# Performance work log

Hardware: AMD Instinct MI355X
Metric: run time of the kernel (lower is better)

## Reference

```python
import jax, jax.numpy as jnp
import numpy as np

B, N, OBS = 512, 64, 256
H1, H2 = 4, 4
D = 128            # embed/key dim (d_k_1 = d_k_2 = 128)
O1 = D // H1       # 32, per-head value dim stage 1
O2 = D // H2       # 32, per-head value dim stage 2
IN2 = O1 * H1      # 128, input dim to stage 2
FOUT = 16          # final_output_dim


def setup_inputs() -> dict:
    key = jax.random.key(0)
    ks = jax.random.split(key, 22)
    g = lambda k, shp: (jax.random.normal(k, shp, dtype=jnp.float32) * 0.05)
    inp = {
        "states": jax.random.normal(ks[0], (B, N, OBS), dtype=jnp.float32),
        # stage 1 per-head params, stacked over heads
        "E1_w": g(ks[1], (H1, D, OBS)), "E1_b": g(ks[2], (H1, D)),
        "K1_w": g(ks[3], (H1, D, D)),   "K1_b": g(ks[4], (H1, D)),
        "Q1_w": g(ks[5], (H1, D, D)),   "Q1_b": g(ks[6], (H1, D)),
        "V1_w": g(ks[7], (H1, O1, D)),  "V1_b": g(ks[8], (H1, O1)),
        # stage 2 per-head params
        "E2_w": g(ks[9], (H2, D, IN2)), "E2_b": g(ks[10], (H2, D)),
        "K2_w": g(ks[11], (H2, D, D)),  "K2_b": g(ks[12], (H2, D)),
        "Q2_w": g(ks[13], (H2, D, D)),  "Q2_b": g(ks[14], (H2, D)),
        "V2_w": g(ks[15], (H2, O2, D)), "V2_b": g(ks[16], (H2, O2)),
        # final MLP policy head
        "F1_w": g(ks[17], (64, O2 * H2)), "F1_b": g(ks[18], (64,)),
        "F2_w": g(ks[19], (FOUT, 64)),    "F2_b": g(ks[20], (FOUT,)),
    }
    return inp


def _attn_block(x, Ew, Eb, Kw, Kb, Qw, Qb, Vw, Vb, d_k):
    # x: [B,N,I]; all head loops batched via leading head axis h
    se = jax.nn.leaky_relu(jnp.einsum('bni,hdi->hbnd', x, Ew) + Eb[:, None, None, :])  # [h,B,N,D]
    k = jnp.einsum('hbnd,hed->hbne', se, Kw) + Kb[:, None, None, :]
    q = jnp.einsum('hbnd,hed->hbne', se, Qw) + Qb[:, None, None, :]
    w = jax.nn.softmax(jnp.einsum('hbne,hbme->hbnm', q, k) / jnp.sqrt(jnp.float32(d_k)), axis=-1)  # [h,B,N,N]
    v = jax.nn.leaky_relu(jnp.einsum('hbnd,hod->hbno', se, Vw) + Vb[:, None, None, :])  # [h,B,N,O]
    att = jnp.einsum('hbnm,hbmo->hbno', w, v)
    h, b, n, o = att.shape
    return jnp.transpose(att, (1, 2, 0, 3)).reshape(b, n, h * o), w


def reference(states, E1_w, E1_b, K1_w, K1_b, Q1_w, Q1_b, V1_w, V1_b,
              E2_w, E2_b, K2_w, K2_b, Q2_w, Q2_b, V2_w, V2_b,
              F1_w, F1_b, F2_w, F2_b):
    x1, w1 = _attn_block(states, E1_w, E1_b, K1_w, K1_b, Q1_w, Q1_b, V1_w, V1_b, D)
    x2, w2 = _attn_block(x1, E2_w, E2_b, K2_w, K2_b, Q2_w, Q2_b, V2_w, V2_b, D)
    h = jax.nn.leaky_relu(jnp.einsum('bnf,of->bno', x2, F1_w) + F1_b)
    policy = jax.nn.softmax(jnp.einsum('bno,po->bnp', h, F2_w) + F2_b, axis=-1)
    return policy, w1, w2
```

## Files before the change

kernel.cpp:

```cpp
#include <hip/hip_runtime.h>

typedef __attribute__((ext_vector_type(8))) short short8;
typedef __attribute__((ext_vector_type(4))) short short4v;
typedef __attribute__((ext_vector_type(4))) float f32x4;

#define MFMA(a, b, c) __builtin_amdgcn_mfma_f32_16x16x32_bf16((a), (b), (c), 0, 0, 0)

__device__ __forceinline__ short f2bf(float f) {
    union { float f; unsigned u; } v; v.f = f;
    unsigned r = v.u + 0x7fffu + ((v.u >> 16) & 1u);
    return (short)(r >> 16);
}
__device__ __forceinline__ float bf2f(short s) {
    union { unsigned u; float f; } v; v.u = ((unsigned)(unsigned short)s) << 16; return v.f;
}

struct ConvArgs { const float* src[10]; int end[10]; };

__global__ __launch_bounds__(256) void convert_weights_kernel(ConvArgs a, short* __restrict__ dst) {
    int i4 = blockIdx.x * 256 + threadIdx.x;
    int seg = 0;
#pragma unroll
    for (int s = 0; s < 9; s++) seg += (i4 >= a.end[s]) ? 1 : 0;
    int base = (seg == 0) ? 0 : a.end[seg - 1];
    float4 v = ((const float4*)a.src[seg])[i4 - base];
    short4v o; o.x = f2bf(v.x); o.y = f2bf(v.y); o.z = f2bf(v.z); o.w = f2bf(v.w);
    *(short4v*)(dst + (size_t)i4 * 4) = o;
}

#define KQ_LD  136
#define VT_LD  72
#define W_LD   72
#define OFF_K  0
#define OFF_Q  8704
#define OFF_SE 17408
#define OFF_VT 17408
#define OFF_W  8704
#define W32_LD 68
#define SMEM_SHORTS 26112

template<int IN, bool XF32>
__global__ __launch_bounds__(256, 3) void attn_stage_kernel(
    const void* __restrict__ xin,
    const short* __restrict__ Ew, const float* __restrict__ Eb,
    const short* __restrict__ Kw, const float* __restrict__ Kb,
    const short* __restrict__ Qw, const float* __restrict__ Qb,
    const short* __restrict__ Vw, const float* __restrict__ Vb,
    float* __restrict__ w_out,
    short* __restrict__ x_out)
{
    __shared__ short sm[SMEM_SHORTS];
    const int tid  = threadIdx.x;
    const int b    = blockIdx.x & 511;
    const int h    = blockIdx.x >> 9;
    const int wv   = tid >> 6;
    const int lane = tid & 63;
    const int quad = lane >> 4;
    const int l16  = lane & 15;
    const int XLD  = IN + 8;
    constexpr int NK1 = IN / 32;

    if constexpr (XF32) {
        const float* xb = (const float*)xin + (size_t)b * 64 * IN;
#pragma unroll
        for (int r = 0; r < IN / 16; r++) {
            int f4 = tid + 256 * r;
            int row = f4 / (IN / 4), c4 = f4 % (IN / 4);
            float4 v = ((const float4*)xb)[f4];
            short4v o; o.x = f2bf(v.x); o.y = f2bf(v.y); o.z = f2bf(v.z); o.w = f2bf(v.w);
            *(short4v*)&sm[row * XLD + c4 * 4] = o;
        }
    } else {
        const short* xb = (const short*)xin + (size_t)b * 64 * IN;
#pragma unroll
        for (int r = 0; r < IN / 32; r++) {
            int f8 = tid + 256 * r;
            int row = f8 / (IN / 8), c8 = f8 % (IN / 8);
            short8 v = *(const short8*)(xb + (size_t)f8 * 8);
            *(short8*)&sm[row * XLD + c8 * 8] = v;
        }
    }

    short8 ebf[NK1 * 2];
    {
        const short* ewh = Ew + (size_t)h * 128 * IN;
#pragma unroll
        for (int k0i = 0; k0i < NK1; k0i++)
#pragma unroll
            for (int j = 0; j < 2; j++)
                ebf[k0i * 2 + j] = *(const short8*)(ewh + (size_t)(wv * 32 + j * 16 + l16) * IN + k0i * 32 + quad * 8);
    }
    __syncthreads();

    short8 kbf[8];

    {
        f32x4 acc[4][2];
#pragma unroll
        for (int j = 0; j < 2; j++) {
            float bv = Eb[h * 128 + wv * 32 + j * 16 + l16];
            f32x4 c = {bv, bv, bv, bv};
#pragma unroll
            for (int i = 0; i < 4; i++) acc[i][j] = c;
        }
#pragma unroll
        for (int k0i = 0; k0i < NK1; k0i++) {
            short8 a[4];
#pragma unroll
            for (int i = 0; i < 4; i++)
                a[i] = *(const short8*)&sm[(i * 16 + l16) * XLD + k0i * 32 + quad * 8];
#pragma unroll
            for (int i = 0; i < 4; i++)
#pragma unroll
                for (int j = 0; j < 2; j++)
                    acc[i][j] = MFMA(a[i], ebf[k0i * 2 + j], acc[i][j]);
        }
        {
            const short* kwh = Kw + (size_t)h * 128 * 128;
#pragma unroll
            for (int k0i = 0; k0i < 4; k0i++)
#pragma unroll
                for (int j = 0; j < 2; j++)
                    kbf[k0i * 2 + j] = *(const short8*)(kwh + (size_t)(wv * 32 + j * 16 + l16) * 128 + k0i * 32 + quad * 8);
        }
#pragma unroll
        for (int i = 0; i < 4; i++)
#pragma unroll
            for (int j = 0; j < 2; j++)
#pragma unroll
                for (int r = 0; r < 4; r++) {
                    float v = acc[i][j][r];
                    v = (v >= 0.f) ? v : 0.01f * v;
                    sm[OFF_SE + (i * 16 + quad * 4 + r) * KQ_LD + wv * 32 + j * 16 + l16] = f2bf(v);
                }
    }
    __syncthreads();

    f32x4 vacc[2];
    {
        short8 qbf[8];
        const short* qwh = Qw + (size_t)h * 128 * 128;
#pragma unroll
        for (int k0i = 0; k0i < 4; k0i++)
#pragma unroll
            for (int j = 0; j < 2; j++)
                qbf[k0i * 2 + j] = *(const short8*)(qwh + (size_t)(wv * 32 + j * 16 + l16) * 128 + k0i * 32 + quad * 8);
        f32x4 kacc[4][2], qacc[4][2];
#pragma unroll
        for (int j = 0; j < 2; j++) {
            float kb = Kb[h * 128 + wv * 32 + j * 16 + l16];
            float qb = Qb[h * 128 + wv * 32 + j * 16 + l16];
            f32x4 kc = {kb, kb, kb, kb}, qc = {qb, qb, qb, qb};
#pragma unroll
            for (int i = 0; i < 4; i++) { kacc[i][j] = kc; qacc[i][j] = qc; }
        }
#pragma unroll
        for (int k0i = 0; k0i < 4; k0i++) {
            short8 a[4];
#pragma unroll
            for (int i = 0; i < 4; i++)
                a[i] = *(const short8*)&sm[OFF_SE + (i * 16 + l16) * KQ_LD + k0i * 32 + quad * 8];
#pragma unroll
            for (int i = 0; i < 4; i++)
#pragma unroll
                for (int j = 0; j < 2; j++) {
                    kacc[i][j] = MFMA(a[i], kbf[k0i * 2 + j], kacc[i][j]);
                    qacc[i][j] = MFMA(a[i], qbf[k0i * 2 + j], qacc[i][j]);
                }
        }
#pragma unroll
        for (int i = 0; i < 4; i++)
#pragma unroll
            for (int j = 0; j < 2; j++)
#pragma unroll
                for (int r = 0; r < 4; r++) {
                    int row = i * 16 + quad * 4 + r, col = wv * 32 + j * 16 + l16;
                    sm[OFF_K + row * KQ_LD + col] = f2bf(kacc[i][j][r]);
                    sm[OFF_Q + row * KQ_LD + col] = f2bf(qacc[i][j][r]);
                }
        const short* vwh = Vw + (size_t)h * 32 * 128;
        const int n0v = (wv >> 1) * 16, mrow = (wv & 1) * 32;
        short8 vbf[4];
#pragma unroll
        for (int k0i = 0; k0i < 4; k0i++)
            vbf[k0i] = *(const short8*)(vwh + (size_t)(n0v + l16) * 128 + k0i * 32 + quad * 8);
        float vb = Vb[h * 32 + n0v + l16];
        vacc[0] = (f32x4){vb, vb, vb, vb}; vacc[1] = vacc[0];
#pragma unroll
        for (int k0i = 0; k0i < 4; k0i++) {
            short8 a0 = *(const short8*)&sm[OFF_SE + (mrow + l16) * KQ_LD + k0i * 32 + quad * 8];
            short8 a1 = *(const short8*)&sm[OFF_SE + (mrow + 16 + l16) * KQ_LD + k0i * 32 + quad * 8];
            vacc[0] = MFMA(a0, vbf[k0i], vacc[0]);
            vacc[1] = MFMA(a1, vbf[k0i], vacc[1]);
        }
    }
    __syncthreads();

    {
        const int n0v = (wv >> 1) * 16, mrow = (wv & 1) * 32;
#pragma unroll
        for (int i = 0; i < 2; i++)
#pragma unroll
            for (int r = 0; r < 4; r++) {
                float v = vacc[i][r];
                v = (v >= 0.f) ? v : 0.01f * v;
                sm[OFF_VT + (n0v + l16) * VT_LD + mrow + i * 16 + quad * 4 + r] = f2bf(v);
            }
    }

    f32x4 lacc[4];
#pragma unroll
    for (int jj = 0; jj < 4; jj++) lacc[jj] = (f32x4){0.f, 0.f, 0.f, 0.f};
#pragma unroll
    for (int k0 = 0; k0 < 128; k0 += 32) {
        short8 a = *(const short8*)&sm[OFF_Q + (wv * 16 + l16) * KQ_LD + k0 + quad * 8];
#pragma unroll
        for (int jj = 0; jj < 4; jj++) {
            short8 b8 = *(const short8*)&sm[OFF_K + (jj * 16 + l16) * KQ_LD + k0 + quad * 8];
            lacc[jj] = MFMA(a, b8, lacc[jj]);
        }
    }
    __syncthreads();

    {
        const float scale = 0.08838834764831845f;
        float* w32 = (float*)sm;
        float mx[4], inv[4];
#pragma unroll
        for (int r = 0; r < 4; r++) {
            float m = lacc[0][r];
#pragma unroll
            for (int jj = 1; jj < 4; jj++) m = fmaxf(m, lacc[jj][r]);
#pragma unroll
            for (int s = 1; s < 16; s <<= 1) m = fmaxf(m, __shfl_xor(m, s, 16));
            mx[r] = m;
        }
        float sum[4] = {0.f, 0.f, 0.f, 0.f};
#pragma unroll
        for (int jj = 0; jj < 4; jj++)
#pragma unroll
            for (int r = 0; r < 4; r++) {
                float e = __expf((lacc[jj][r] - mx[r]) * scale);
                lacc[jj][r] = e; sum[r] += e;
            }
#pragma unroll
        for (int r = 0; r < 4; r++) {
#pragma unroll
            for (int s = 1; s < 16; s <<= 1) sum[r] += __shfl_xor(sum[r], s, 16);
            inv[r] = 1.0f / sum[r];
        }
#pragma unroll
        for (int r = 0; r < 4; r++) {
            int row = wv * 16 + quad * 4 + r;
#pragma unroll
            for (int jj = 0; jj < 4; jj++) {
                float wval = lacc[jj][r] * inv[r];
                w32[row * W32_LD + jj * 16 + l16] = wval;
                sm[OFF_W + row * W_LD + jj * 16 + l16] = f2bf(wval);
            }
        }
    }
    __syncthreads();

    {
        const float* w32 = (const float*)sm;
        float* wbase = w_out + ((size_t)(h * 512 + b)) * 64 * 64;
#pragma unroll
        for (int s = 0; s < 4; s++) {
            int idx = tid + 256 * s;
            int row = idx >> 4, c4 = (idx & 15) * 4;
            f32x4 v = *(const f32x4*)&w32[row * W32_LD + c4];
            __builtin_nontemporal_store(v, (f32x4*)(wbase + idx * 4));
        }
    }

    {
        f32x4 aacc[2]; aacc[0] = (f32x4){0.f, 0.f, 0.f, 0.f}; aacc[1] = aacc[0];
#pragma unroll
        for (int k0 = 0; k0 < 64; k0 += 32) {
            short8 a = *(const short8*)&sm[OFF_W + (wv * 16 + l16) * W_LD + k0 + quad * 8];
#pragma unroll
            for (int j = 0; j < 2; j++) {
                short8 b8 = *(const short8*)&sm[OFF_VT + (j * 16 + l16) * VT_LD + k0 + quad * 8];
                aacc[j] = MFMA(a, b8, aacc[j]);
            }
        }
        short* xob = x_out + (size_t)b * 64 * 128;
#pragma unroll
        for (int j = 0; j < 2; j++)
#pragma unroll
            for (int r = 0; r < 4; r++)
                xob[(size_t)(wv * 16 + quad * 4 + r) * 128 + h * 32 + j * 16 + l16] = f2bf(aacc[j][r]);
    }
}

#define H_LD 72
__global__ __launch_bounds__(256)
void final_mlp_mfma_kernel(const short* __restrict__ x2,
                           const short* __restrict__ F1wb,
                           const float* __restrict__ F1b,
                           const short* __restrict__ F2wb,
                           const float* __restrict__ F2b,
                           float* __restrict__ policy)
{
    __shared__ short hsm[4][16 * H_LD];
    const int tid  = threadIdx.x;
    const int wv   = tid >> 6;
    const int lane = tid & 63;
    const int quad = lane >> 4;
    const int l16  = lane & 15;
    const int rowbase = blockIdx.x * 64 + wv * 16;

    short8 a[4];
    const short* xrow = x2 + (size_t)(rowbase + l16) * 128;
#pragma unroll
    for (int k = 0; k < 4; k++) a[k] = *(const short8*)(xrow + k * 32 + quad * 8);
    f32x4 acc[4];
#pragma unroll
    for (int j = 0; j < 4; j++) { float bv = F1b[j * 16 + l16]; acc[j] = (f32x4){bv, bv, bv, bv}; }
#pragma unroll
    for (int k = 0; k < 4; k++)
#pragma unroll
        for (int j = 0; j < 4; j++) {
            short8 b8 = *(const short8*)(F1wb + (size_t)(j * 16 + l16) * 128 + k * 32 + quad * 8);
            acc[j] = MFMA(a[k], b8, acc[j]);
        }
    short* hh = &hsm[wv][0];
#pragma unroll
    for (int j = 0; j < 4; j++)
#pragma unroll
        for (int r = 0; r < 4; r++) {
            float v = acc[j][r];
            v = (v >= 0.f) ? v : 0.01f * v;
            hh[(quad * 4 + r) * H_LD + j * 16 + l16] = f2bf(v);
        }
    __syncthreads();

    f32x4 lg;
    { float bv = F2b[l16]; lg = (f32x4){bv, bv, bv, bv}; }
#pragma unroll
    for (int k = 0; k < 2; k++) {
        short8 a2 = *(const short8*)(hh + l16 * H_LD + k * 32 + quad * 8);
        short8 b8 = *(const short8*)(F2wb + (size_t)l16 * 64 + k * 32 + quad * 8);
        lg = MFMA(a2, b8, lg);
    }
#pragma unroll
    for (int r = 0; r < 4; r++) {
        float m = lg[r];
        m = fmaxf(m, __shfl_xor(m, 1, 16));
        m = fmaxf(m, __shfl_xor(m, 2, 16));
        m = fmaxf(m, __shfl_xor(m, 4, 16));
        m = fmaxf(m, __shfl_xor(m, 8, 16));
        float e = __expf(lg[r] - m);
        float s = e;
        s += __shfl_xor(s, 1, 16);
        s += __shfl_xor(s, 2, 16);
        s += __shfl_xor(s, 4, 16);
        s += __shfl_xor(s, 8, 16);
        policy[(size_t)(rowbase + quad * 4 + r) * 16 + l16] = e / s;
    }
}

extern "C" void kernel_launch(void* const* d_in, const int* in_sizes, int n_in,
                              void* d_out, int out_size, void* d_ws, size_t ws_size,
                              hipStream_t stream) {
    const float* states = (const float*)d_in[0];
    const float* E1w = (const float*)d_in[1];  const float* E1b = (const float*)d_in[2];
    const float* K1w = (const float*)d_in[3];  const float* K1b = (const float*)d_in[4];
    const float* Q1w = (const float*)d_in[5];  const float* Q1b = (const float*)d_in[6];
    const float* V1w = (const float*)d_in[7];  const float* V1b = (const float*)d_in[8];
    const float* E2w = (const float*)d_in[9];  const float* E2b = (const float*)d_in[10];
    const float* K2w = (const float*)d_in[11]; const float* K2b = (const float*)d_in[12];
    const float* Q2w = (const float*)d_in[13]; const float* Q2b = (const float*)d_in[14];
    const float* V2w = (const float*)d_in[15]; const float* V2b = (const float*)d_in[16];
    const float* F1w = (const float*)d_in[17]; const float* F1b = (const float*)d_in[18];
    const float* F2w = (const float*)d_in[19]; const float* F2b = (const float*)d_in[20];

    float* out    = (float*)d_out;
    float* policy = out;
    float* w1     = out + 512 * 64 * 16;
    float* w2     = w1 + 4 * 512 * 64 * 64;

    short* wsb = (short*)d_ws;
    short* x1b = wsb;
    short* x2b = wsb + 4194304;
    short* wts = wsb + 8388608;
    short* wE1 = wts;            short* wK1 = wts + 131072;
    short* wQ1 = wts + 196608;   short* wV1 = wts + 262144;
    short* wE2 = wts + 278528;   short* wK2 = wts + 344064;
    short* wQ2 = wts + 409600;   short* wV2 = wts + 475136;
    short* wF1 = wts + 491520;   short* wF2 = wts + 499712;

    ConvArgs ca;
    ca.src[0] = E1w; ca.src[1] = K1w; ca.src[2] = Q1w; ca.src[3] = V1w;
    ca.src[4] = E2w; ca.src[5] = K2w; ca.src[6] = Q2w; ca.src[7] = V2w;
    ca.src[8] = F1w; ca.src[9] = F2w;
    ca.end[0] = 32768;  ca.end[1] = 49152;  ca.end[2] = 65536;  ca.end[3] = 69632;
    ca.end[4] = 86016;  ca.end[5] = 102400; ca.end[6] = 118784; ca.end[7] = 122880;
    ca.end[8] = 124928; ca.end[9] = 125184;
    convert_weights_kernel<<<489, 256, 0, stream>>>(ca, wts);

    attn_stage_kernel<256, true><<<2048, 256, 0, stream>>>(
        (const void*)states, wE1, E1b, wK1, K1b, wQ1, Q1b, wV1, V1b, w1, x1b);
    attn_stage_kernel<128, false><<<2048, 256, 0, stream>>>(
        (const void*)x1b, wE2, E2b, wK2, K2b, wQ2, Q2b, wV2, V2b, w2, x2b);
    final_mlp_mfma_kernel<<<512, 256, 0, stream>>>(x2b, wF1, F1b, wF2, F2b, policy);
}
```

Before: 219.3 us.

## Fold K and Q projections into a single precomputed Kw^T·Qw matrix per head

Precomputes M = Kw^T Qw (plus a Qb·Kw row) per head in a prep kernel, so logits become (se·M^T)·se^T plus a per-key bias term. Terms that are constant per query row (Kb, and Qb·Kb) are dropped because softmax cancels them. This removes one of the two 128x128 projections and the separate K/Q shared-memory buffers. Shared memory drops enough to raise occupancy from 3 to 4 blocks per CU. The cost is a serial fp32 matrix product in the prep kernel and extra bf16 rounding of the fused matrix, which can change numerical accuracy.

```diff
diff --git a/kernel.cpp b/kernel.cpp
--- a/kernel.cpp
+++ b/kernel.cpp
@@ -15,36 +15,75 @@
     union { unsigned u; float f; } v; v.u = ((unsigned)(unsigned short)s) << 16; return v.f;
 }
 
-struct ConvArgs { const float* src[10]; int end[10]; };
-
-__global__ __launch_bounds__(256) void convert_weights_kernel(ConvArgs a, short* __restrict__ dst) {
-    int i4 = blockIdx.x * 256 + threadIdx.x;
-    int seg = 0;
-#pragma unroll
-    for (int s = 0; s < 9; s++) seg += (i4 >= a.end[s]) ? 1 : 0;
-    int base = (seg == 0) ? 0 : a.end[seg - 1];
-    float4 v = ((const float4*)a.src[seg])[i4 - base];
-    short4v o; o.x = f2bf(v.x); o.y = f2bf(v.y); o.z = f2bf(v.z); o.w = f2bf(v.w);
-    *(short4v*)(dst + (size_t)i4 * 4) = o;
-}
-
-#define KQ_LD  136
+struct PrepArgs {
+    const float* csrc[6]; int cend[6];
+    const float* K1w; const float* Q1w; const float* Q1b;
+    const float* K2w; const float* Q2w; const float* Q2b;
+};
+
+__global__ __launch_bounds__(256) void prep_kernel(PrepArgs a, short* __restrict__ dstW,
+                                                   short* __restrict__ M1, short* __restrict__ M2) {
+    const int blk = blockIdx.x, t = threadIdx.x;
+    if (blk < 233) {
+        int i4 = blk * 256 + t;
+        int seg = 0;
+#pragma unroll
+        for (int s = 0; s < 5; s++) seg += (i4 >= a.cend[s]) ? 1 : 0;
+        int base = (seg == 0) ? 0 : a.cend[seg - 1];
+        float4 v = ((const float4*)a.csrc[seg])[i4 - base];
+        short4v o; o.x = f2bf(v.x); o.y = f2bf(v.y); o.z = f2bf(v.z); o.w = f2bf(v.w);
+        *(short4v*)(dstW + (size_t)i4 * 4) = o;
+    } else {
+        int mi = blk - 233;
+        int mat = mi / 9, rg = mi % 9;
+        int s = mat >> 2, h = mat & 3;
+        const float* Kw = s ? a.K2w : a.K1w;
+        const float* Qw = s ? a.Q2w : a.Q1w;
+        const float* Qb = s ? a.Q2b : a.Q1b;
+        short* Mt = (s ? M2 : M1) + h * 144 * 128;
+        int r  = rg * 16 + (t >> 4);
+        int d0 = (t & 15) * 8;
+        float acc[8];
+#pragma unroll
+        for (int j = 0; j < 8; j++) acc[j] = 0.f;
+        const float* kw = Kw + (size_t)h * 16384;
+        if (r < 128) {
+            const float* qw = Qw + (size_t)h * 16384;
+            for (int e = 0; e < 128; e++) {
+                float kv = kw[e * 128 + r];
+                const float* q = qw + e * 128 + d0;
+#pragma unroll
+                for (int j = 0; j < 8; j++) acc[j] = fmaf(kv, q[j], acc[j]);
+            }
+        } else if (r == 128) {
+            const float* qb = Qb + h * 128;
+            for (int e = 0; e < 128; e++) {
+                float qv = qb[e];
+                const float* kk = kw + e * 128 + d0;
+#pragma unroll
+                for (int j = 0; j < 8; j++) acc[j] = fmaf(qv, kk[j], acc[j]);
+            }
+        }
+#pragma unroll
+        for (int j = 0; j < 8; j++) Mt[r * 128 + d0 + j] = f2bf(acc[j]);
+    }
+}
+
+#define SE_LD  136
+#define T_LD   136
 #define VT_LD  72
 #define W_LD   72
-#define OFF_K  0
-#define OFF_Q  8704
-#define OFF_SE 17408
-#define OFF_VT 17408
-#define OFF_W  8704
 #define W32_LD 68
-#define SMEM_SHORTS 26112
+#define R1     8704
+#define R2     17408
+#define D2OFF  19712
+#define SMEM_SHORTS 19840
 
 template<int IN, bool XF32>
-__global__ __launch_bounds__(256, 3) void attn_stage_kernel(
+__global__ __launch_bounds__(256, 4) void attn_stage_kernel(
     const void* __restrict__ xin,
     const short* __restrict__ Ew, const float* __restrict__ Eb,
-    const short* __restrict__ Kw, const float* __restrict__ Kb,
-    const short* __restrict__ Qw, const float* __restrict__ Qb,
+    const short* __restrict__ Mt,
     const short* __restrict__ Vw, const float* __restrict__ Vb,
     float* __restrict__ w_out,
     short* __restrict__ x_out)
@@ -57,27 +96,28 @@
     const int lane = tid & 63;
     const int quad = lane >> 4;
     const int l16  = lane & 15;
-    const int XLD  = IN + 8;
-    constexpr int NK1 = IN / 32;
+    constexpr int NK1   = IN / 32;
+    constexpr int XLD   = IN + 8;
+    constexpr int XBASE = XF32 ? 0 : R1;
 
     if constexpr (XF32) {
         const float* xb = (const float*)xin + (size_t)b * 64 * IN;
 #pragma unroll
-        for (int r = 0; r < IN / 16; r++) {
+        for (int r = 0; r < 16; r++) {
             int f4 = tid + 256 * r;
-            int row = f4 / (IN / 4), c4 = f4 % (IN / 4);
+            int row = f4 >> 6, c4 = (f4 & 63) * 4;
             float4 v = ((const float4*)xb)[f4];
             short4v o; o.x = f2bf(v.x); o.y = f2bf(v.y); o.z = f2bf(v.z); o.w = f2bf(v.w);
-            *(short4v*)&sm[row * XLD + c4 * 4] = o;
+            *(short4v*)&sm[row * XLD + c4] = o;
         }
     } else {
         const short* xb = (const short*)xin + (size_t)b * 64 * IN;
 #pragma unroll
-        for (int r = 0; r < IN / 32; r++) {
+        for (int r = 0; r < 4; r++) {
             int f8 = tid + 256 * r;
-            int row = f8 / (IN / 8), c8 = f8 % (IN / 8);
+            int row = f8 >> 4, c8 = (f8 & 15) * 8;
             short8 v = *(const short8*)(xb + (size_t)f8 * 8);
-            *(short8*)&sm[row * XLD + c8 * 8] = v;
+            *(short8*)&sm[XBASE + row * 136 + c8] = v;
         }
     }
 
@@ -92,7 +132,7 @@
     }
     __syncthreads();
 
-    short8 kbf[8];
+    short8 mbf[8], xbf[4], vbf[4];
 
     {
         f32x4 acc[4][2];
@@ -108,7 +148,7 @@
             short8 a[4];
 #pragma unroll
             for (int i = 0; i < 4; i++)
-                a[i] = *(const short8*)&sm[(i * 16 + l16) * XLD + k0i * 32 + quad * 8];
+                a[i] = *(const short8*)&sm[XBASE + (i * 16 + l16) * XLD + k0i * 32 + quad * 8];
 #pragma unroll
             for (int i = 0; i < 4; i++)
 #pragma unroll
@@ -116,13 +156,17 @@
                     acc[i][j] = MFMA(a[i], ebf[k0i * 2 + j], acc[i][j]);
         }
         {
-            const short* kwh = Kw + (size_t)h * 128 * 128;
-#pragma unroll
-            for (int k0i = 0; k0i < 4; k0i++)
+            const short* mth = Mt + (size_t)h * 144 * 128;
+#pragma unroll
+            for (int k0i = 0; k0i < 4; k0i++) {
 #pragma unroll
                 for (int j = 0; j < 2; j++)
-                    kbf[k0i * 2 + j] = *(const short8*)(kwh + (size_t)(wv * 32 + j * 16 + l16) * 128 + k0i * 32 + quad * 8);
-        }
+                    mbf[k0i * 2 + j] = *(const short8*)(mth + (size_t)(wv * 32 + j * 16 + l16) * 128 + k0i * 32 + quad * 8);
+                xbf[k0i] = *(const short8*)(mth + (size_t)(128 + l16) * 128 + k0i * 32 + quad * 8);
+                vbf[k0i] = *(const short8*)(Vw + (size_t)h * 32 * 128 + (size_t)(((wv >> 1) * 16) + l16) * 128 + k0i * 32 + quad * 8);
+            }
+        }
+        if constexpr (XF32) __syncthreads();
 #pragma unroll
         for (int i = 0; i < 4; i++)
 #pragma unroll
@@ -131,92 +175,86 @@
                 for (int r = 0; r < 4; r++) {
                     float v = acc[i][j][r];
                     v = (v >= 0.f) ? v : 0.01f * v;
-                    sm[OFF_SE + (i * 16 + quad * 4 + r) * KQ_LD + wv * 32 + j * 16 + l16] = f2bf(v);
+                    sm[(i * 16 + quad * 4 + r) * SE_LD + wv * 32 + j * 16 + l16] = f2bf(v);
                 }
     }
     __syncthreads();
 
-    f32x4 vacc[2];
-    {
-        short8 qbf[8];
-        const short* qwh = Qw + (size_t)h * 128 * 128;
-#pragma unroll
-        for (int k0i = 0; k0i < 4; k0i++)
-#pragma unroll
-            for (int j = 0; j < 2; j++)
-                qbf[k0i * 2 + j] = *(const short8*)(qwh + (size_t)(wv * 32 + j * 16 + l16) * 128 + k0i * 32 + quad * 8);
-        f32x4 kacc[4][2], qacc[4][2];
-#pragma unroll
-        for (int j = 0; j < 2; j++) {
-            float kb = Kb[h * 128 + wv * 32 + j * 16 + l16];
-            float qb = Qb[h * 128 + wv * 32 + j * 16 + l16];
-            f32x4 kc = {kb, kb, kb, kb}, qc = {qb, qb, qb, qb};
-#pragma unroll
-            for (int i = 0; i < 4; i++) { kacc[i][j] = kc; qacc[i][j] = qc; }
+    {
+        f32x4 tacc[4][2], dacc[4];
+#pragma unroll
+        for (int i = 0; i < 4; i++) {
+#pragma unroll
+            for (int j = 0; j < 2; j++) tacc[i][j] = (f32x4){0.f, 0.f, 0.f, 0.f};
+            dacc[i] = (f32x4){0.f, 0.f, 0.f, 0.f};
         }
 #pragma unroll
         for (int k0i = 0; k0i < 4; k0i++) {
             short8 a[4];
 #pragma unroll
             for (int i = 0; i < 4; i++)
-                a[i] = *(const short8*)&sm[OFF_SE + (i * 16 + l16) * KQ_LD + k0i * 32 + quad * 8];
+                a[i] = *(const short8*)&sm[(i * 16 + l16) * SE_LD + k0i * 32 + quad * 8];
 #pragma unroll
             for (int i = 0; i < 4; i++)
 #pragma unroll
-                for (int j = 0; j < 2; j++) {
-                    kacc[i][j] = MFMA(a[i], kbf[k0i * 2 + j], kacc[i][j]);
-                    qacc[i][j] = MFMA(a[i], qbf[k0i * 2 + j], qacc[i][j]);
-                }
+                for (int j = 0; j < 2; j++)
+                    tacc[i][j] = MFMA(a[i], mbf[k0i * 2 + j], tacc[i][j]);
+            if (wv == 0) {
+#pragma unroll
+                for (int i = 0; i < 4; i++) dacc[i] = MFMA(a[i], xbf[k0i], dacc[i]);
+            }
         }
 #pragma unroll
         for (int i = 0; i < 4; i++)
 #pragma unroll
             for (int j = 0; j < 2; j++)
 #pragma unroll
-                for (int r = 0; r < 4; r++) {
-                    int row = i * 16 + quad * 4 + r, col = wv * 32 + j * 16 + l16;
-                    sm[OFF_K + row * KQ_LD + col] = f2bf(kacc[i][j][r]);
-                    sm[OFF_Q + row * KQ_LD + col] = f2bf(qacc[i][j][r]);
-                }
-        const short* vwh = Vw + (size_t)h * 32 * 128;
+                for (int r = 0; r < 4; r++)
+                    sm[R1 + (i * 16 + quad * 4 + r) * T_LD + wv * 32 + j * 16 + l16] = f2bf(tacc[i][j][r]);
+        if (wv == 0 && l16 == 0) {
+            float* d2f = (float*)&sm[D2OFF];
+#pragma unroll
+            for (int i = 0; i < 4; i++)
+#pragma unroll
+                for (int r = 0; r < 4; r++)
+                    d2f[i * 16 + quad * 4 + r] = dacc[i][r];
+        }
         const int n0v = (wv >> 1) * 16, mrow = (wv & 1) * 32;
-        short8 vbf[4];
-#pragma unroll
-        for (int k0i = 0; k0i < 4; k0i++)
-            vbf[k0i] = *(const short8*)(vwh + (size_t)(n0v + l16) * 128 + k0i * 32 + quad * 8);
         float vb = Vb[h * 32 + n0v + l16];
-        vacc[0] = (f32x4){vb, vb, vb, vb}; vacc[1] = vacc[0];
+        f32x4 vacc[2]; vacc[0] = (f32x4){vb, vb, vb, vb}; vacc[1] = vacc[0];
 #pragma unroll
         for (int k0i = 0; k0i < 4; k0i++) {
-            short8 a0 = *(const short8*)&sm[OFF_SE + (mrow + l16) * KQ_LD + k0i * 32 + quad * 8];
-            short8 a1 = *(const short8*)&sm[OFF_SE + (mrow + 16 + l16) * KQ_LD + k0i * 32 + quad * 8];
+            short8 a0 = *(const short8*)&sm[(mrow + l16) * SE_LD + k0i * 32 + quad * 8];
+            short8 a1 = *(const short8*)&sm[(mrow + 16 + l16) * SE_LD + k0i * 32 + quad * 8];
             vacc[0] = MFMA(a0, vbf[k0i], vacc[0]);
             vacc[1] = MFMA(a1, vbf[k0i], vacc[1]);
         }
-    }
-    __syncthreads();
-
-    {
-        const int n0v = (wv >> 1) * 16, mrow = (wv & 1) * 32;
 #pragma unroll
         for (int i = 0; i < 2; i++)
 #pragma unroll
             for (int r = 0; r < 4; r++) {
                 float v = vacc[i][r];
                 v = (v >= 0.f) ? v : 0.01f * v;
-                sm[OFF_VT + (n0v + l16) * VT_LD + mrow + i * 16 + quad * 4 + r] = f2bf(v);
-            }
-    }
-
+                sm[R2 + (n0v + l16) * VT_LD + mrow + i * 16 + quad * 4 + r] = f2bf(v);
+            }
+    }
+    __syncthreads();
+
+    float d2v[4];
+    {
+        const float* d2f = (const float*)&sm[D2OFF];
+#pragma unroll
+        for (int jj = 0; jj < 4; jj++) d2v[jj] = d2f[jj * 16 + l16];
+    }
     f32x4 lacc[4];
 #pragma unroll
     for (int jj = 0; jj < 4; jj++) lacc[jj] = (f32x4){0.f, 0.f, 0.f, 0.f};
 #pragma unroll
     for (int k0 = 0; k0 < 128; k0 += 32) {
-        short8 a = *(const short8*)&sm[OFF_Q + (wv * 16 + l16) * KQ_LD + k0 + quad * 8];
+        short8 a = *(const short8*)&sm[R1 + (wv * 16 + l16) * T_LD + k0 + quad * 8];
 #pragma unroll
         for (int jj = 0; jj < 4; jj++) {
-            short8 b8 = *(const short8*)&sm[OFF_K + (jj * 16 + l16) * KQ_LD + k0 + quad * 8];
+            short8 b8 = *(const short8*)&sm[(jj * 16 + l16) * SE_LD + k0 + quad * 8];
             lacc[jj] = MFMA(a, b8, lacc[jj]);
         }
     }
@@ -225,6 +263,10 @@
     {
         const float scale = 0.08838834764831845f;
         float* w32 = (float*)sm;
+#pragma unroll
+        for (int jj = 0; jj < 4; jj++)
+#pragma unroll
+            for (int r = 0; r < 4; r++) lacc[jj][r] += d2v[jj];
         float mx[4], inv[4];
 #pragma unroll
         for (int r = 0; r < 4; r++) {
@@ -256,7 +298,7 @@
             for (int jj = 0; jj < 4; jj++) {
                 float wval = lacc[jj][r] * inv[r];
                 w32[row * W32_LD + jj * 16 + l16] = wval;
-                sm[OFF_W + row * W_LD + jj * 16 + l16] = f2bf(wval);
+                sm[R1 + row * W_LD + jj * 16 + l16] = f2bf(wval);
             }
         }
     }
@@ -278,10 +320,10 @@
         f32x4 aacc[2]; aacc[0] = (f32x4){0.f, 0.f, 0.f, 0.f}; aacc[1] = aacc[0];
 #pragma unroll
         for (int k0 = 0; k0 < 64; k0 += 32) {
-            short8 a = *(const short8*)&sm[OFF_W + (wv * 16 + l16) * W_LD + k0 + quad * 8];
+            short8 a = *(const short8*)&sm[R1 + (wv * 16 + l16) * W_LD + k0 + quad * 8];
 #pragma unroll
             for (int j = 0; j < 2; j++) {
-                short8 b8 = *(const short8*)&sm[OFF_VT + (j * 16 + l16) * VT_LD + k0 + quad * 8];
+                short8 b8 = *(const short8*)&sm[R2 + (j * 16 + l16) * VT_LD + k0 + quad * 8];
                 aacc[j] = MFMA(a, b8, aacc[j]);
             }
         }
@@ -366,11 +408,11 @@
                               hipStream_t stream) {
     const float* states = (const float*)d_in[0];
     const float* E1w = (const float*)d_in[1];  const float* E1b = (const float*)d_in[2];
-    const float* K1w = (const float*)d_in[3];  const float* K1b = (const float*)d_in[4];
+    const float* K1w = (const float*)d_in[3];
     const float* Q1w = (const float*)d_in[5];  const float* Q1b = (const float*)d_in[6];
     const float* V1w = (const float*)d_in[7];  const float* V1b = (const float*)d_in[8];
     const float* E2w = (const float*)d_in[9];  const float* E2b = (const float*)d_in[10];
-    const float* K2w = (const float*)d_in[11]; const float* K2b = (const float*)d_in[12];
+    const float* K2w = (const float*)d_in[11];
     const float* Q2w = (const float*)d_in[13]; const float* Q2b = (const float*)d_in[14];
     const float* V2w = (const float*)d_in[15]; const float* V2b = (const float*)d_in[16];
     const float* F1w = (const float*)d_in[17]; const float* F1b = (const float*)d_in[18];
@@ -385,24 +427,23 @@
     short* x1b = wsb;
     short* x2b = wsb + 4194304;
     short* wts = wsb + 8388608;
-    short* wE1 = wts;            short* wK1 = wts + 131072;
-    short* wQ1 = wts + 196608;   short* wV1 = wts + 262144;
-    short* wE2 = wts + 278528;   short* wK2 = wts + 344064;
-    short* wQ2 = wts + 409600;   short* wV2 = wts + 475136;
-    short* wF1 = wts + 491520;   short* wF2 = wts + 499712;
-
-    ConvArgs ca;
-    ca.src[0] = E1w; ca.src[1] = K1w; ca.src[2] = Q1w; ca.src[3] = V1w;
-    ca.src[4] = E2w; ca.src[5] = K2w; ca.src[6] = Q2w; ca.src[7] = V2w;
-    ca.src[8] = F1w; ca.src[9] = F2w;
-    ca.end[0] = 32768;  ca.end[1] = 49152;  ca.end[2] = 65536;  ca.end[3] = 69632;
-    ca.end[4] = 86016;  ca.end[5] = 102400; ca.end[6] = 118784; ca.end[7] = 122880;
-    ca.end[8] = 124928; ca.end[9] = 125184;
-    convert_weights_kernel<<<489, 256, 0, stream>>>(ca, wts);
+    short* wE1 = wts;            short* wV1 = wts + 131072;
+    short* wE2 = wts + 147456;   short* wV2 = wts + 212992;
+    short* wF1 = wts + 229376;   short* wF2 = wts + 237568;
+    short* M1  = wts + 238592;   short* M2  = M1 + 73728;
+
+    PrepArgs pa;
+    pa.csrc[0] = E1w; pa.csrc[1] = V1w; pa.csrc[2] = E2w;
+    pa.csrc[3] = V2w; pa.csrc[4] = F1w; pa.csrc[5] = F2w;
+    pa.cend[0] = 32768; pa.cend[1] = 36864; pa.cend[2] = 53248;
+    pa.cend[3] = 57344; pa.cend[4] = 59392; pa.cend[5] = 59648;
+    pa.K1w = K1w; pa.Q1w = Q1w; pa.Q1b = Q1b;
+    pa.K2w = K2w; pa.Q2w = Q2w; pa.Q2b = Q2b;
+    prep_kernel<<<305, 256, 0, stream>>>(pa, wts, M1, M2);
 
     attn_stage_kernel<256, true><<<2048, 256, 0, stream>>>(
-        (const void*)states, wE1, E1b, wK1, K1b, wQ1, Q1b, wV1, V1b, w1, x1b);
+        (const void*)states, wE1, E1b, M1, wV1, V1b, w1, x1b);
     attn_stage_kernel<128, false><<<2048, 256, 0, stream>>>(
-        (const void*)x1b, wE2, E2b, wK2, K2b, wQ2, Q2b, wV2, V2b, w2, x2b);
+        (const void*)x1b, wE2, E2b, M2, wV2, V2b, w2, x2b);
     final_mlp_mfma_kernel<<<512, 256, 0, stream>>>(x2b, wF1, F1b, wF2, F2b, policy);
 }
```

Result: slower. 230.2 us (+5.0%).
